# Kernel tuning notes

Hardware: AMD Instinct MI355X
Metric: run time of the kernel (lower is better)

## Reference

```python
import jax, jax.numpy as jnp
import numpy as np
from jax import lax

B, T, C, H, W = 2, 5, 2, 128, 256
E, M, L = 64, 16, 4  # embedding_dim, n_fno_modes, n_fno_layers
EPS = 1e-5


def conv1x1(x, w, b):
    # x: [N, I, H, W], w: [O, I], b: [O]
    return jnp.einsum('nihw,oi->nohw', x, w) + b[None, :, None, None]


def conv3x3(x, w, b):
    # x: [N, I, H, W], w: [O, I, 3, 3]
    y = lax.conv_general_dilated(x, w, window_strides=(1, 1), padding='SAME',
                                 dimension_numbers=('NCHW', 'OIHW', 'NCHW'))
    return y + b[None, :, None, None]


def instance_norm(x):
    # InstanceNorm2d(affine=False): normalize over H,W per (n, c), biased var
    mu = jnp.mean(x, axis=(2, 3), keepdims=True)
    var = jnp.var(x, axis=(2, 3), keepdims=True)
    return (x - mu) * lax.rsqrt(var + EPS)


def upsample2x_nearest(x):
    return jnp.repeat(jnp.repeat(x, 2, axis=2), 2, axis=3)


def resize_nearest(x, out_h, out_w):
    # torch F.interpolate mode='nearest': idx = floor(i * in / out)
    in_h, in_w = x.shape[2], x.shape[3]
    hi = (jnp.arange(out_h) * in_h) // out_h
    wi = (jnp.arange(out_w) * in_w) // out_w
    return x[:, :, hi, :][:, :, :, wi]


def fno_layer(x, wr, wi, cw, cb):
    # x: [N, E, H, W]; wr/wi: [2, E, E, M, M]; cw: [E, E]; cb: [E]
    h, w = x.shape[2], x.shape[3]
    coeff = jnp.fft.rfft2(x, axes=(2, 3), norm='ortho')  # [N, E, H, W//2+1]
    w0 = wr[0] + 1j * wi[0]
    w1 = wr[1] + 1j * wi[1]
    out = jnp.zeros_like(coeff)
    out = out.at[:, :, :M, :M].set(
        jnp.einsum('nixy,ioxy->noxy', coeff[:, :, :M, :M], w0))
    out = out.at[:, :, -M:, :M].set(
        jnp.einsum('nixy,ioxy->noxy', coeff[:, :, -M:, :M], w1))
    spec = jnp.fft.irfft2(out, s=(h, w), axes=(2, 3), norm='ortho')
    return jax.nn.gelu(conv1x1(x, cw, cb) + spec, approximate=False)


def setup_inputs() -> dict:
    key = jax.random.key(0)
    ks = jax.random.split(key, 10)
    s = 0.02
    return {
        'sensor_value': jax.random.normal(ks[0], (B, T, C, H, W), jnp.float32),
        'updim_w': 0.3 * jax.random.normal(ks[1], (E, C), jnp.float32),
        'updim_b': jnp.zeros((E,), jnp.float32),
        'smooth_w': 0.04 * jax.random.normal(ks[2], (E, E, 3, 3), jnp.float32),
        'smooth_b': jnp.zeros((E,), jnp.float32),
        'fno_wr': s * jax.random.normal(ks[3], (L, 2, E, E, M, M), jnp.float32),
        'fno_wi': s * jax.random.normal(ks[4], (L, 2, E, E, M, M), jnp.float32),
        'fno_cw': 0.1 * jax.random.normal(ks[5], (L, E, E), jnp.float32),
        'fno_cb': jnp.zeros((L, E), jnp.float32),
        'downdim_w': 0.1 * jax.random.normal(ks[6], (C, E), jnp.float32),
        'downdim_b': jnp.zeros((C,), jnp.float32),
    }


def reference(sensor_value, updim_w, updim_b, smooth_w, smooth_b,
              fno_wr, fno_wi, fno_cw, fno_cb, downdim_w, downdim_b):
    b, t, c, h, w = sensor_value.shape
    x = sensor_value.reshape(b * t, c, h, w)
    x = conv1x1(x, updim_w, updim_b)
    x = upsample2x_nearest(x)
    x = jax.nn.gelu(instance_norm(conv3x3(x, smooth_w, smooth_b)), approximate=False)
    x = resize_nearest(x, H, W)
    for l in range(L):
        x = fno_layer(x, fno_wr[l], fno_wi[l], fno_cw[l], fno_cb[l])
    x = conv1x1(x, downdim_w, downdim_b)
    return x.reshape(b, t, c, H, W)
```

## Files before the change

### kernel.cpp

```cpp
#include <hip/hip_runtime.h>
#include <math.h>

#define PI_D 3.14159265358979323846


typedef _Float16 h8 __attribute__((ext_vector_type(8)));
typedef _Float16 h4v __attribute__((ext_vector_type(4)));
typedef float f16v __attribute__((ext_vector_type(16)));

__device__ __forceinline__ float gelu_f(float v){
  return 0.5f*v*(1.0f + erff(v*0.70710678118654752440f));
}

__device__ __forceinline__ int fsw_c(int w){ return (w ^ (w >> 3)) & 7; }

__global__ __launch_bounds__(256) void k_tables_fold(float* __restrict__ twFwH, float* __restrict__ twBwH,
                                                     _Float16* __restrict__ Tspec, _Float16* __restrict__ TdftW,
                                                     const float* __restrict__ smw, const float* __restrict__ upw,
                                                     const float* __restrict__ upb, float* __restrict__ Keff){
  int bid = blockIdx.x;
  if (bid < 96){
    int id = bid*256 + threadIdx.x;
    if (id < 4096){
      int h = id >> 5, m = id & 31;
      int xm = (m < 16) ? m : (96 + m);
      double ang = -2.0*PI_D*(double)((xm*h) & 127)/128.0;
      twFwH[id*2]   = (float)cos(ang);
      twFwH[id*2+1] = (float)sin(ang);
    } else if (id < 8192){
      int j = id - 4096;
      int h = j >> 5, m = j & 31;
      int xm = (m < 16) ? m : (96 + m);
      double ang = 2.0*PI_D*(double)((xm*h) & 127)/128.0;
      twBwH[j*2]   = (float)cos(ang);
      twBwH[j*2+1] = (float)sin(ang);
    } else if (id < 16384){
      int j = id - 8192;
      int w = j >> 5, kk = j & 31;
      int y = kk >> 1;
      double ang = 2.0*PI_D*(double)((w*y) & 255)/256.0;
      double v = (kk & 1) ? -sin(ang) : cos(ang);
      Tspec[j] = (_Float16)v;
    } else if (id < 24576){
      int j = id - 16384;
      int y2 = j >> 8, w = j & 255;
      int y = y2 >> 1;
      double ang = -2.0*PI_D*(double)((w*y) & 255)/256.0;
      double v = (y2 & 1) ? sin(ang) : cos(ang);
      TdftW[j] = (_Float16)v;
    }
  } else {
    int id = (bid-96)*256 + threadIdx.x;
    if (id >= 1024) return;
    int o = id >> 4, rs = (id >> 2) & 3, tap = id & 3;
    int r = rs >> 1, s = rs & 1, a = tap >> 1, b = tap & 1;
    int klo = (r==0) ? (a==0?0:1) : (a==0?0:2);
    int khi = (r==0) ? (a==0?0:2) : (a==0?1:2);
    int llo = (s==0) ? (b==0?0:1) : (b==0?0:2);
    int lhi = (s==0) ? (b==0?0:2) : (b==0?1:2);
    float a0=0.f, a1=0.f, ab=0.f;
    for (int i=0;i<64;++i){
      float t = 0.f;
      for (int kh=klo; kh<=khi; ++kh)
        for (int kw=llo; kw<=lhi; ++kw)
          t += smw[((size_t)o*64+i)*9 + kh*3+kw];
      a0 += t*upw[i*2];
      a1 += t*upw[i*2+1];
      ab += t*upb[i];
    }
    *(float4*)(Keff + o*64 + (rs*4+tap)*4) = make_float4(a0, a1, ab, 0.f);
  }
}

__global__ __launch_bounds__(256) void k_transW(const float* __restrict__ wr, const float* __restrict__ wi,
                                                unsigned* __restrict__ Wt){
  __shared__ unsigned P[64*257];
  int lb = blockIdx.x;
  int i = lb & 63, blk = (lb>>6)&1, l = lb>>7;
  int tid = threadIdx.x;
  size_t sbase = (size_t)l*2097152 + (size_t)blk*1048576 + (size_t)i*16384 + tid;
  for (int o=0;o<64;++o){
    float a = wr[sbase + (size_t)o*256];
    float b = wi[sbase + (size_t)o*256];
    union { unsigned u; _Float16 h[2]; } pk;
    pk.h[0] = (_Float16)a; pk.h[1] = (_Float16)b;
    P[o*257 + tid] = pk.u;
  }
  __syncthreads();
  int o = tid & 63, g = tid >> 6;
  size_t dbase = (size_t)(l*2+blk)*1048576;
  for (int it=0; it<64; ++it){
    int my = g*64 + it;
    Wt[dbase + (size_t)my*4096 + i*64 + o] = P[o*257 + my];
  }
}

__global__ __launch_bounds__(512) void k_corrbnd(const float* __restrict__ sv, float* __restrict__ Rpart,
                                                 float* __restrict__ Bnd){
  __shared__ float SH[3120];
  int bid = blockIdx.x;
  int tid = threadIdx.x;
  if (bid < 320){
    int band = bid & 31, n = bid >> 5;
    int u0 = band*4;
    for (int t = tid; t < 3120; t += 512){
      int ch = t / 1560; int rem = t - ch*1560; int rr = rem / 260; int ci = rem - rr*260;
      int row = u0 - 1 + rr, col = ci - 1;
      float v = 0.f;
      if (row >= 0 && row < 128 && col >= 0 && col < 256)
        v = sv[((size_t)(n*2+ch)*128 + row)*256 + col];
      SH[(ch*6+rr)*260 + ci] = v;
    }
    __syncthreads();

    int lane = tid & 63, wv = tid >> 6;
    int c  = (wv<4) ? (wv>>1) : ((wv<6) ? (wv-4) : 2);
    int c2 = (wv<4) ? (wv&1)  : ((wv<6) ? 2 : (wv-6));
    float acc[9];
    #pragma unroll
    for (int k=0;k<9;++k) acc[k]=0.f;

    for (int r=0;r<4;++r){
      int u = u0 + r, lu = r + 1;
      for (int cb=0;cb<4;++cb){
        int v = cb*64 + lane;
        float f = (c==2) ? 1.f : SH[(c*6+lu)*260 + 1+v];
        #pragma unroll
        for (int dr=-1;dr<=1;++dr){
          int ur = u + dr;
          float rko = (ur>=0 && ur<128) ? 1.f : 0.f;
          #pragma unroll
          for (int dc=-1;dc<=1;++dc){
            float g;
            if (c2==2){
              int vc = v + dc;
              g = rko * ((vc>=0 && vc<256) ? 1.f : 0.f);
            } else {
              g = SH[(c2*6+lu+dr)*260 + 1+v+dc];
            }
            acc[(dr+1)*3 + dc+1] += f*g;
          }
        }
      }
    }
    #pragma unroll
    for (int k=0;k<9;++k){
      float v = acc[k];
      for (int off=32; off; off>>=1) v += __shfl_xor(v, off);
      if (lane==0) Rpart[((size_t)(n*32+band)*8 + wv)*9 + k] = v;
    }
  } else {
    int n = bid - 320;
    for (int t = tid; t < 3120; t += 512){
      int e = t/780; int rem = t - e*780; int ch = rem/260; int i = rem - ch*260;
      int idx = i - 1;
      int len = (e<2) ? 256 : 128;
      float v = 0.f;
      if (idx >= 0 && idx < len){
        if (ch==2) v = 1.f;
        else {
          int row = (e==0) ? 0 : (e==1) ? 127 : idx;
          int col = (e==2) ? 0 : (e==3) ? 255 : idx;
          v = sv[((size_t)(n*2+ch)*128 + row)*256 + col];
        }
      }
      SH[(e*3+ch)*260 + i] = v;
    }
    __syncthreads();
    if (tid < 108){
      int e = tid/27; int rem = tid - e*27; int pair = rem/3; int lag = rem%3 - 1;
      int c = pair/3, c2 = pair%3;
      int len = (e<2) ? 256 : 128;
      float a = 0.f;
      for (int i=0;i<len;++i) a += SH[(e*3+c)*260 + 1+i]*SH[(e*3+c2)*260 + 1+i+lag];
      Bnd[n*144 + tid] = a;
    } else if (tid < 144){
      int t = tid - 108; int corner = t/9; int pair = t - corner*9;
      int c = pair/3, c2 = pair%3;
      int e = (corner<2) ? 0 : 1;
      int idx = (corner&1) ? 255 : 0;
      Bnd[n*144 + tid] = SH[(e*3+c)*260 + 1+idx]*SH[(e*3+c2)*260 + 1+idx];
    }
  }
}

__global__ __launch_bounds__(256) void k_stats3(const float* __restrict__ Rpart, const float* __restrict__ Bnd,
                                                const float* __restrict__ Keff, float* __restrict__ stats){
  __shared__ float R[9][9];
  __shared__ float BL[4][9][3];
  __shared__ float CR[4][9];
  __shared__ float M[4][12][12];
  int n = blockIdx.x, tid = threadIdx.x;

  if (tid < 72){
    int wv = tid/9, k = tid - (tid/9)*9;
    double s = 0.0;
    for (int b=0;b<32;++b) s += (double)Rpart[((size_t)(n*32+b)*8 + wv)*9 + k];
    int c  = (wv<4) ? (wv>>1) : ((wv<6) ? (wv-4) : 2);
    int c2 = (wv<4) ? (wv&1)  : ((wv<6) ? 2 : (wv-6));
    R[c*3+c2][k] = (float)s;
  } else if (tid < 81){
    int k = tid - 72; int dr = k/3 - 1, dc = k%3 - 1;
    R[8][k] = (float)((128 - (dr<0?-dr:dr)) * (256 - (dc<0?-dc:dc)));
  }
  if (tid < 108){
    int e = tid/27, rem = tid - (tid/27)*27;
    BL[e][rem/3][rem%3] = Bnd[n*144 + tid];
  } else if (tid < 144){
    int t = tid - 108;
    CR[t/9][t - (t/9)*9] = Bnd[n*144 + tid];
  }
  __syncthreads();

  for (int t = tid; t < 576; t += 256){
    int rs = t/144; int rem = t - rs*144; int i = rem/12, j = rem - (rem/12)*12;
    int ab = i/3,  c  = i - ab*3,  a  = ab>>1, b  = ab&1;
    int ab2 = j/3, c2 = j - ab2*3, a2 = ab2>>1, b2 = ab2&1;
    int r = rs>>1, s = rs&1;
    int dr = a2 - a, dc = b2 - b;
    int pair = c*3 + c2;
    float g = R[pair][(dr+1)*3 + (dc+1)];
    if (r==1 && a==1 && a2==1) g -= BL[0][pair][dc+1];
    if (r==0 && a==0 && a2==0) g -= BL[1][pair][dc+1];
    if (s==1 && b==1 && b2==1) g -= BL[2][pair][dr+1];
    if (s==0 && b==0 && b2==0) g -= BL[3][pair][dr+1];
    bool rowc = (a==a2) && ((r==1 && a==1) || (r==0 && a==0));
    bool colc = (b==b2) && ((s==1 && b==1) || (s==0 && b==0));
    if (rowc && colc){
      int corner = ((r==1)?0:2) + ((s==1)?0:1);
      g += CR[corner][pair];
    }
    M[rs][i][j] = g;
  }
  __syncthreads();

  if (tid < 64){
    int o = tid;
    double S1 = 0.0, S2 = 0.0;
    for (int rs=0; rs<4; ++rs){
      float w[12];
      #pragma unroll
      for (int ab=0; ab<4; ++ab){
        float4 kv = *(const float4*)(Keff + o*64 + (rs*4+ab)*4);
        w[ab*3+0] = kv.x; w[ab*3+1] = kv.y; w[ab*3+2] = kv.z;
      }
      #pragma unroll
      for (int i=0;i<12;++i){
        double ti = 0.0;
        #pragma unroll
        for (int j=0;j<12;++j) ti += (double)M[rs][i][j]*(double)w[j];
        S2 += (double)w[i]*ti;
      }
      #pragma unroll
      for (int ab=0; ab<4; ++ab)
        #pragma unroll
        for (int c=0;c<3;++c)
          S1 += (double)w[ab*3+c]*(double)M[rs][ab*3+c][ab*3+2];
    }
    double mu  = S1 / 131072.0;
    double var = S2 / 131072.0 - mu*mu;
    stats[(n*64+o)*2]   = (float)mu;
    stats[(n*64+o)*2+1] = (float)(1.0/sqrt(var + 1e-5));
  }
}

__global__ __launch_bounds__(1024, 8) void k_convnorm(const float* __restrict__ sv,
                                                      const float* __restrict__ Keff,
                                                      const float* __restrict__ stats,
                                                      const _Float16* __restrict__ TdftW,
                                                      _Float16* __restrict__ act,
                                                      float* __restrict__ Cy){
  __shared__ __align__(16) _Float16 Lh[40960];
  _Float16* gL  = Lh;
  _Float16* TdL = Lh + 16384;
  float*    P   = (float*)(Lh + 24576);
  float*    SV  = P;
  int bid = blockIdx.x;
  int p = bid & 127, n = bid >> 7;
  int tid = threadIdx.x;
  for (int t = tid; t < 1032; t += 1024){
    int dr = t / 516;
    int rem = t - dr*516;
    int ch = rem / 258;
    int ci = rem - ch*258;
    int row = p - 1 + dr;
    int col = ci - 1;
    float v = 0.f;
    if (row >= 0 && col >= 0 && col < 256)
      v = sv[((size_t)(n*2+ch)*128 + row)*256 + col];
    SV[(dr*2+ch)*260 + ci] = v;
  }
  {
    int y2 = tid & 31, ws = (tid >> 5)*8;
    const _Float16* src = TdftW + y2*256 + ws;
    h8 v = *(const h8*)src;
    int chunk = (ws>>3) ^ (y2 & 7);
    *(h8*)(TdL + y2*256 + chunk*8) = v;
  }
  __syncthreads();

  int q = tid & 255;
  int og = __builtin_amdgcn_readfirstlane(tid >> 8);
  float x0[4], x1[4], ib[4];
  float rowok0 = (p>0)?1.f:0.f;
  float colok0 = (q>0)?1.f:0.f;
  #pragma unroll
  for (int a=0;a<2;++a)
    #pragma unroll
    for (int b=0;b<2;++b){
      x0[a*2+b] = SV[(a*2+0)*260 + q + b];
      x1[a*2+b] = SV[(a*2+1)*260 + q + b];
      ib[a*2+b] = (a==0?rowok0:1.f) * (b==0?colok0:1.f);
    }

  union { _Float16 g16[16]; h8 gv8[2]; } U;
  int q3 = q>>3, q7 = q&7;
  #pragma unroll
  for (int oi=0; oi<16; ++oi){
    int o = og*16 + oi;
    const float4* kp = (const float4*)(Keff + o*64);
    float y = 0.f;
    #pragma unroll
    for (int t=0;t<4;++t){
      float4 kv = kp[t];
      y += kv.x*x0[t] + kv.y*x1[t] + kv.z*ib[t];
    }
    float mu = stats[(n*64+o)*2], istd = stats[(n*64+o)*2+1];
    _Float16 gh = (_Float16)gelu_f((y - mu)*istd);
    U.g16[oi] = gh;
    gL[o*256 + ((q3 ^ (o & 7))*8) + q7] = gh;
  }
  {
    _Float16* ap = act + (((size_t)(n*128+p)*256 + q)*64 + og*16);
    *(h8*)ap = U.gv8[0];
    *(h8*)(ap+8) = U.gv8[1];
  }
  __syncthreads();

  int lane = tid & 63;
  int l31 = lane & 31, l5 = lane >> 5;
  int w0i = tid >> 6;
  if (w0i < 8){
    int mt2 = w0i & 1, kq = w0i >> 1;
    int ocol = mt2*32 + l31;
    f16v acc2;
    #pragma unroll
    for (int j=0;j<16;++j) acc2[j] = 0.f;
    #pragma unroll
    for (int ks=0;ks<4;++ks){
      int kb = (kq*4+ks)*16 + l5*8;
      h8 af2 = *(const h8*)(gL  + ocol*256 + (((kb>>3) ^ (ocol & 7))*8));
      h8 bf2 = *(const h8*)(TdL + l31*256  + (((kb>>3) ^ (l31 & 7))*8));
      acc2 = __builtin_amdgcn_mfma_f32_32x32x16_f16(bf2, af2, acc2, 0,0,0);
    }
    #pragma unroll
    for (int j=0;j<16;++j){
      int y2 = (j&3) + 8*(j>>2) + 4*l5;
      P[w0i*1024 + y2*32 + l31] = acc2[j];
    }
  }
  __syncthreads();
  {
    int yy = tid >> 6, o = tid & 63, mt2 = o >> 5, o31 = o & 31;
    float re = P[(0*2+mt2)*1024 + (2*yy)*32 + o31]   + P[(1*2+mt2)*1024 + (2*yy)*32 + o31]
             + P[(2*2+mt2)*1024 + (2*yy)*32 + o31]   + P[(3*2+mt2)*1024 + (2*yy)*32 + o31];
    float im = P[(0*2+mt2)*1024 + (2*yy+1)*32 + o31] + P[(1*2+mt2)*1024 + (2*yy+1)*32 + o31]
             + P[(2*2+mt2)*1024 + (2*yy+1)*32 + o31] + P[(3*2+mt2)*1024 + (2*yy+1)*32 + o31];
    *(float2*)(Cy + (((size_t)(n*16+yy)*128 + p)*64 + o)*2) = make_float2(re, im);
  }
}

__global__ __launch_bounds__(256) void k_specAB(const float* __restrict__ Cy,
                                                const float* __restrict__ twF,
                                                const unsigned* __restrict__ Wt,
                                                float* __restrict__ MS, int l){
  __shared__ float CO[8*64*2];
  int bid = blockIdx.x;
  int mq = bid / 160;
  int pid = bid - mq*160;
  int y = pid & 15, n = pid >> 4;
  int tid = threadIdx.x;
  int lane = tid & 63;
  int wv = __builtin_amdgcn_readfirstlane(tid >> 6);

  {
    int m0 = mq*8 + wv*2;
    const float* cyb = Cy + (((size_t)(n*16+y)*128)*64 + lane)*2;
    const float* tf = twF + m0*2;
    float ar0=0.f, ai0=0.f, ar1=0.f, ai1=0.f;
    for (int h=0; h<128; ++h){
      float2 c = *(const float2*)(cyb + h*128);
      const float* tp = tf + h*64;
      float t0r = tp[0], t0i = tp[1], t1r = tp[2], t1i = tp[3];
      ar0 += t0r*c.x - t0i*c.y; ai0 += t0r*c.y + t0i*c.x;
      ar1 += t1r*c.x - t1i*c.y; ai1 += t1r*c.y + t1i*c.x;
    }
    int mm = wv*2;
    *(float2*)(CO + (mm*64 + lane)*2)     = make_float2(ar0, ai0);
    *(float2*)(CO + ((mm+1)*64 + lane)*2) = make_float2(ar1, ai1);
  }
  __syncthreads();

  {
    float f = (y==0) ? (1.f/32768.f) : (2.f/32768.f);
    #pragma unroll
    for (int t2=0; t2<2; ++t2){
      int mm = wv*2 + t2;
      int m = mq*8 + mm;
      int blk = m >> 4, mloc = m & 15;
      int my = mloc*16 + y;
      const unsigned* wb = Wt + ((size_t)((l*2+blk)*256 + my))*4096 + lane;
      float mr = 0.f, mi = 0.f;
      for (int i=0;i<64;++i){
        float2 cc = *(const float2*)(CO + (mm*64 + i)*2);
        union { unsigned u; _Float16 h[2]; } pk;
        pk.u = wb[(size_t)i*64];
        float wr_f = (float)pk.h[0], wi_f = (float)pk.h[1];
        mr += cc.x*wr_f - cc.y*wi_f;
        mi += cc.x*wi_f + cc.y*wr_f;
      }
      *(float2*)(MS + (((size_t)(n*16+y)*32 + m)*64 + lane)*2) = make_float2(mr*f, mi*f);
    }
  }
}

__global__ __launch_bounds__(1024, 8) void k_combine_mfma(const _Float16* __restrict__ act_in,
                                                          const float* __restrict__ MS,
                                                          const _Float16* __restrict__ Tspec,
                                                          const _Float16* __restrict__ TdftW,
                                                          const float* __restrict__ twB,
                                                          const float* __restrict__ cw,
                                                          const float* __restrict__ cb,
                                                          const float* __restrict__ wd,
                                                          const float* __restrict__ bd,
                                                          _Float16* __restrict__ act_out,
                                                          float* __restrict__ Cy,
                                                          float* __restrict__ outp,
                                                          int flags){
  __shared__ __align__(16) _Float16 Lh[40960];
  _Float16* Bx = Lh;
  _Float16* At = Lh + 32768;
  int tid = threadIdx.x;
  int h = blockIdx.x & 127, n = blockIdx.x >> 7;

  int wA = tid >> 2, ksg = tid & 3;
  const _Float16* asrc = act_in + (((size_t)(n*128+h)*256 + wA)*64 + ksg*16);
  h8 av0 = *(const h8*)asrc;
  h8 av1 = *(const h8*)(asrc + 8);

  int o_g = tid & 63;
  int yv = __builtin_amdgcn_readfirstlane(tid >> 6);
  float gr = 0.f, gi = 0.f;
  {
    const float* ms = MS + (size_t)(n*16+yv)*4096 + o_g*2;
    const float* tb = twB + h*64;
    #pragma unroll 4
    for (int m=0;m<32;++m){
      float tr = tb[m*2], ti = tb[m*2+1];
      float2 mo = *(const float2*)(ms + m*128);
      gr += tr*mo.x - ti*mo.y;
      gi += tr*mo.y + ti*mo.x;
    }
  }

  {
    int fw = fsw_c(wA);
    *(h8*)(Bx + wA*128 + ((ksg*2)   ^ fw)*8) = av0;
    *(h8*)(Bx + wA*128 + ((ksg*2+1) ^ fw)*8) = av1;
  }
  if (tid < 512){
    int o = tid >> 3, seg = (tid & 7)*8;
    float4 c0 = *(const float4*)(cw + o*64 + seg);
    float4 c1 = *(const float4*)(cw + o*64 + seg + 4);
    h8 v;
    v[0]=(_Float16)c0.x; v[1]=(_Float16)c0.y; v[2]=(_Float16)c0.z; v[3]=(_Float16)c0.w;
    v[4]=(_Float16)c1.x; v[5]=(_Float16)c1.y; v[6]=(_Float16)c1.z; v[7]=(_Float16)c1.w;
    int ch0 = (seg>>3) ^ (o & 7);
    *(h8*)(At + o*128 + ch0*8) = v;
  } else {
    int t5 = tid - 512;
    int w = t5 >> 1, half = t5 & 1;
    const _Float16* tp = Tspec + w*32 + half*16;
    int fw = fsw_c(w);
    #pragma unroll
    for (int c=0;c<2;++c){
      h8 v = *(const h8*)(tp + c*8);
      int cc = half*2 + c;
      *(h8*)(Bx + w*128 + ((8 + cc) ^ fw)*8) = v;
    }
  }
  {
    int kk0 = 64 + 2*yv;
    At[o_g*128 + (((kk0>>3) ^ (o_g & 7))*8) + (kk0 & 7)] = (_Float16)gr;
    int kk1 = kk0 + 1;
    At[o_g*128 + (((kk1>>3) ^ (o_g & 7))*8) + (kk1 & 7)] = (_Float16)gi;
  }
  __syncthreads();

  int lane = tid & 63;
  int l31 = lane & 31, l5 = lane >> 5;
  int w0i = tid >> 6;
  int mt = w0i & 1, ng = w0i >> 1;
  int o_lane = mt*32 + l31;

  h8 af[6];
  #pragma unroll
  for (int ks=0;ks<6;++ks){
    int kb = ks*16 + l5*8;
    int chunk = (kb>>3) ^ (o_lane & 7);
    af[ks] = *(const h8*)(At + o_lane*128 + chunk*8);
  }

  f16v acc;
  #pragma unroll
  for (int j=0;j<16;++j) acc[j] = cb[mt*32 + (j&3) + 8*(j>>2) + 4*l5];

  int wcol = ng*32 + l31;
  {
    const _Float16* bbase = Bx + wcol*128;
    int wf = fsw_c(wcol);
    #pragma unroll
    for (int ks=0;ks<6;++ks){
      int kb = ks*16 + l5*8;
      int chunk = (kb>>3) ^ wf;
      h8 bf = *(const h8*)(bbase + chunk*8);
      acc = __builtin_amdgcn_mfma_f32_32x32x16_f16(af[ks], bf, acc, 0,0,0);
    }
  }

  float gvv[16];
  #pragma unroll
  for (int j=0;j<16;++j) gvv[j] = gelu_f(acc[j]);

  if (flags != 2){
    _Float16* ab = act_out + (((size_t)(n*128+h)*256 + wcol)*64 + mt*32 + 4*l5);
    #pragma unroll
    for (int g=0;g<4;++g){
      h4v v4;
      v4[0]=(_Float16)gvv[g*4+0]; v4[1]=(_Float16)gvv[g*4+1];
      v4[2]=(_Float16)gvv[g*4+2]; v4[3]=(_Float16)gvv[g*4+3];
      *(h4v*)(ab + 8*g) = v4;
    }
  }
  __syncthreads();

  if (flags == 1){
    _Float16* gL  = Lh;
    _Float16* TdL = Lh + 16384;
    {
      int wc3 = wcol >> 3, wc7 = wcol & 7;
      #pragma unroll
      for (int j=0;j<16;++j){
        int o = mt*32 + (j&3) + 8*(j>>2) + 4*l5;
        gL[o*256 + ((wc3 ^ (o & 7))*8) + wc7] = (_Float16)gvv[j];
      }
    }
    {
      int y2 = tid & 31, ws = (tid >> 5)*8;
      const _Float16* src = TdftW + y2*256 + ws;
      h8 v = *(const h8*)src;
      int chunk = (ws>>3) ^ (y2 & 7);
      *(h8*)(TdL + y2*256 + chunk*8) = v;
    }
    __syncthreads();
    float* P = (float*)(Lh + 24576);
    if (w0i < 8){
      int mt2 = w0i & 1, kq = w0i >> 1;
      int ocol = mt2*32 + l31;
      f16v acc2;
      #pragma unroll
      for (int j=0;j<16;++j) acc2[j] = 0.f;
      #pragma unroll
      for (int ks=0;ks<4;++ks){
        int kb = (kq*4+ks)*16 + l5*8;
        h8 af2 = *(const h8*)(gL  + ocol*256 + (((kb>>3) ^ (ocol & 7))*8));
        h8 bf2 = *(const h8*)(TdL + l31*256  + (((kb>>3) ^ (l31 & 7))*8));
        acc2 = __builtin_amdgcn_mfma_f32_32x32x16_f16(bf2, af2, acc2, 0,0,0);
      }
      #pragma unroll
      for (int j=0;j<16;++j){
        int y2 = (j&3) + 8*(j>>2) + 4*l5;
        P[w0i*1024 + y2*32 + l31] = acc2[j];
      }
    }
    __syncthreads();
    {
      int yy = tid >> 6, o = tid & 63, mt2 = o >> 5, o31 = o & 31;
      float re = P[(0*2+mt2)*1024 + (2*yy)*32 + o31]   + P[(1*2+mt2)*1024 + (2*yy)*32 + o31]
               + P[(2*2+mt2)*1024 + (2*yy)*32 + o31]   + P[(3*2+mt2)*1024 + (2*yy)*32 + o31];
      float im = P[(0*2+mt2)*1024 + (2*yy+1)*32 + o31] + P[(1*2+mt2)*1024 + (2*yy+1)*32 + o31]
               + P[(2*2+mt2)*1024 + (2*yy+1)*32 + o31] + P[(3*2+mt2)*1024 + (2*yy+1)*32 + o31];
      *(float2*)(Cy + (((size_t)(n*16+yy)*128 + h)*64 + o)*2) = make_float2(re, im);
    }
  } else {
    float p0=0.f, p1=0.f;
    #pragma unroll
    for (int j=0;j<16;++j){
      int o = mt*32 + (j&3) + 8*(j>>2) + 4*l5;
      p0 += wd[o]*gvv[j];
      p1 += wd[64+o]*gvv[j];
    }
    p0 += __shfl_xor(p0,32);
    p1 += __shfl_xor(p1,32);
    float* red = (float*)(Lh + 32768);
    if (l5 == 0){
      red[wcol*4 + mt*2 + 0] = p0;
      red[wcol*4 + mt*2 + 1] = p1;
    }
    __syncthreads();
    if (tid < 512){
      int ch = tid >> 8, wc = tid & 255;
      float v = red[wc*4 + ch] + red[wc*4 + 2 + ch] + bd[ch];
      outp[(size_t)n*65536 + (size_t)ch*32768 + (size_t)h*256 + wc] = v;
    }
  }
}

extern "C" void kernel_launch(void* const* d_in, const int* in_sizes, int n_in,
                              void* d_out, int out_size, void* d_ws, size_t ws_size,
                              hipStream_t stream) {
  const float* sv  = (const float*)d_in[0];
  const float* upw = (const float*)d_in[1];
  const float* upb = (const float*)d_in[2];
  const float* smw = (const float*)d_in[3];
  const float* smb = (const float*)d_in[4];
  const float* fwr = (const float*)d_in[5];
  const float* fwi = (const float*)d_in[6];
  const float* fcw = (const float*)d_in[7];
  const float* fcb = (const float*)d_in[8];
  const float* ddw = (const float*)d_in[9];
  const float* ddb = (const float*)d_in[10];
  float* out = (float*)d_out;
  (void)smb;

  float* W = (float*)d_ws;
  _Float16* actA = (_Float16*)W;
  _Float16* actB = (_Float16*)(W + 10485760);
  float* Cy    = W + 20971520;
  float* part  = W + 26214400;
  float* stats = W + 28180480;
  float* Keff  = W + 28181760;
  float* twFwH = W + 28185856;
  float* twBwH = W + 28194048;
  _Float16* Tspec = (_Float16*)(W + 28202240);
  _Float16* TdftW = (_Float16*)(W + 28206336);
  unsigned* Wt   = (unsigned*)(W + 28210432);

  float* Rpart = part;
  float* Bnd   = part + 30000;
  float* MS    = part + 65536;

  k_tables_fold<<<100,256,0,stream>>>(twFwH, twBwH, Tspec, TdftW, smw, upw, upb, Keff);
  k_transW<<<512,256,0,stream>>>(fwr, fwi, Wt);
  k_corrbnd<<<330,512,0,stream>>>(sv, Rpart, Bnd);
  k_stats3<<<10,256,0,stream>>>(Rpart, Bnd, Keff, stats);
  k_convnorm<<<1280,1024,0,stream>>>(sv, Keff, stats, TdftW, actA, Cy);

  _Float16* xa = actA; _Float16* xb = actB;
  for (int l=0;l<4;++l){
    k_specAB<<<640,256,0,stream>>>(Cy, twFwH, Wt, MS, l);
    k_combine_mfma<<<1280,1024,0,stream>>>(xa, MS, Tspec, TdftW, twBwH,
                                           fcw + (size_t)l*4096, fcb + (size_t)l*64,
                                           ddw, ddb, xb, Cy, out, (l<3)?1:2);
    _Float16* t = xa; xa = xb; xb = t;
  }
}
```

Measured before the change: 482.4 us.

## Split inverse H-direction spectral transform into separate k_specC kernel

Moves the per-row inverse DFT along H (contracting the 32 retained modes with backward twiddles) out of k_combine_mfma into a new k_specC kernel. k_specC stages the mode spectra in LDS and writes a per-(n,h) G buffer. The combine kernel now loads precomputed values with one float4 per thread instead of running a 32-step loop over global memory at the start of every block. The intent is to shorten the combine kernel's prologue and drop its redundant twiddle loads, at the cost of an extra launch per layer plus writing and reading the G buffer.

```diff
diff --git a/kernel.cpp b/kernel.cpp
--- a/kernel.cpp
+++ b/kernel.cpp
@@ -424,11 +424,47 @@
   }
 }
 
+__global__ __launch_bounds__(256) void k_specC(const float* __restrict__ MS,
+                                               const float* __restrict__ twB,
+                                               float* __restrict__ G){
+  __shared__ float SM[32*64*2];
+  int bid = blockIdx.x;
+  int hq = bid / 160;
+  int pid = bid - hq*160;
+  int y = pid & 15, n = pid >> 4;
+  int tid = threadIdx.x;
+  int lane = tid & 63;
+  int wv = __builtin_amdgcn_readfirstlane(tid >> 6);
+
+  {
+    const float4* src = (const float4*)(MS + ((size_t)(n*16+y)*32)*128);
+    float4* dst = (float4*)SM;
+    #pragma unroll
+    for (int t=0; t<4; ++t) dst[tid + t*256] = src[tid + t*256];
+  }
+  __syncthreads();
+
+  for (int k=0;k<8;++k){
+    int h = hq*32 + wv*8 + k;
+    const float* tb = twB + h*64;
+    float gr=0.f, gi=0.f;
+    #pragma unroll
+    for (int m=0;m<32;++m){
+      float tr = tb[m*2], ti = tb[m*2+1];
+      float2 mo2 = *(const float2*)(SM + (m*64+lane)*2);
+      gr += tr*mo2.x - ti*mo2.y;
+      gi += tr*mo2.y + ti*mo2.x;
+    }
+    size_t gb = (((size_t)(n*128+h)*16 + y)*2)*64 + lane;
+    G[gb]      = gr;
+    G[gb + 64] = gi;
+  }
+}
+
 __global__ __launch_bounds__(1024, 8) void k_combine_mfma(const _Float16* __restrict__ act_in,
-                                                          const float* __restrict__ MS,
+                                                          const float* __restrict__ G,
                                                           const _Float16* __restrict__ Tspec,
                                                           const _Float16* __restrict__ TdftW,
-                                                          const float* __restrict__ twB,
                                                           const float* __restrict__ cw,
                                                           const float* __restrict__ cb,
                                                           const float* __restrict__ wd,
@@ -447,22 +483,6 @@
   const _Float16* asrc = act_in + (((size_t)(n*128+h)*256 + wA)*64 + ksg*16);
   h8 av0 = *(const h8*)asrc;
   h8 av1 = *(const h8*)(asrc + 8);
-
-  int o_g = tid & 63;
-  int yv = __builtin_amdgcn_readfirstlane(tid >> 6);
-  float gr = 0.f, gi = 0.f;
-  {
-    const float* ms = MS + (size_t)(n*16+yv)*4096 + o_g*2;
-    const float* tb = twB + h*64;
-    #pragma unroll 4
-    for (int m=0;m<32;++m){
-      float tr = tb[m*2], ti = tb[m*2+1];
-      float2 mo = *(const float2*)(ms + m*128);
-      gr += tr*mo.x - ti*mo.y;
-      gi += tr*mo.y + ti*mo.x;
-    }
-  }
-
   {
     int fw = fsw_c(wA);
     *(h8*)(Bx + wA*128 + ((ksg*2)   ^ fw)*8) = av0;
@@ -479,7 +499,22 @@
     *(h8*)(At + o*128 + ch0*8) = v;
   } else {
     int t5 = tid - 512;
-    int w = t5 >> 1, half = t5 & 1;
+    const float* gp = G + (size_t)(n*128 + h)*2048 + t5*4;
+    float4 g = *(const float4*)gp;
+    float gvx[4] = {g.x, g.y, g.z, g.w};
+    int idx0 = t5*4;
+    int yc = idx0 >> 6;
+    int o0 = idx0 & 63;
+    int kk = 64 + yc;
+    #pragma unroll
+    for (int j=0;j<4;++j){
+      int o = o0 + j;
+      int chunk = (kk >> 3) ^ (o & 7);
+      At[o*128 + chunk*8 + (kk & 7)] = (_Float16)gvx[j];
+    }
+  }
+  if (tid < 512){
+    int w = tid >> 1, half = tid & 1;
     const _Float16* tp = Tspec + w*32 + half*16;
     int fw = fsw_c(w);
     #pragma unroll
@@ -488,12 +523,6 @@
       int cc = half*2 + c;
       *(h8*)(Bx + w*128 + ((8 + cc) ^ fw)*8) = v;
     }
-  }
-  {
-    int kk0 = 64 + 2*yv;
-    At[o_g*128 + (((kk0>>3) ^ (o_g & 7))*8) + (kk0 & 7)] = (_Float16)gr;
-    int kk1 = kk0 + 1;
-    At[o_g*128 + (((kk1>>3) ^ (o_g & 7))*8) + (kk1 & 7)] = (_Float16)gi;
   }
   __syncthreads();
 
@@ -637,6 +666,7 @@
   _Float16* actA = (_Float16*)W;
   _Float16* actB = (_Float16*)(W + 10485760);
   float* Cy    = W + 20971520;
+  float* G     = W + 23592960;
   float* part  = W + 26214400;
   float* stats = W + 28180480;
   float* Keff  = W + 28181760;
@@ -659,7 +689,8 @@
   _Float16* xa = actA; _Float16* xb = actB;
   for (int l=0;l<4;++l){
     k_specAB<<<640,256,0,stream>>>(Cy, twFwH, Wt, MS, l);
-    k_combine_mfma<<<1280,1024,0,stream>>>(xa, MS, Tspec, TdftW, twBwH,
+    k_specC<<<640,256,0,stream>>>(MS, twBwH, G);
+    k_combine_mfma<<<1280,1024,0,stream>>>(xa, G, Tspec, TdftW,
                                            fcw + (size_t)l*4096, fcb + (size_t)l*64,
                                            ddw, ddb, xb, Cy, out, (l<3)?1:2);
     _Float16* t = xa; xa = xb; xb = t;
```

After: 491.4 us. About the same (+1.9%).
